# Kernel tuning notes

Measured on AMD Instinct MI355X. Metric: run time of the kernel, lower is better.

## Reference

```python
import jax, jax.numpy as jnp
import numpy as np

B, F, D = 16384, 32, 64   # batch, n_continuous_features, input_dim
H = 2 * D                  # hidden = 2*input_dim per the d_hidden spec


def setup_inputs() -> dict:
    key = jax.random.key(0)
    ks = jax.random.split(key, 6)
    s1 = 1.0 / np.sqrt(D).astype(np.float32)
    s2 = 1.0 / np.sqrt(H).astype(np.float32)
    return {
        "X": jax.random.normal(ks[0], (B, F), jnp.float32),
        "r_": jax.random.normal(ks[1], (B, F, D), jnp.float32),
        # stacked per-feature weights (one tiny MLP per continuous column)
        "W1": jax.random.normal(ks[2], (F, D, H), jnp.float32) * s1,
        "b1": jax.random.normal(ks[3], (F, H), jnp.float32) * s1,
        "W2": jax.random.normal(ks[4], (F, H, 1), jnp.float32) * s2,
        "b2": jax.random.normal(ks[5], (F, 1), jnp.float32) * s2,
    }


def reference(X, r_, W1, b1, W2, b2):
    # Per-feature 2-layer MLP (Linear->relu->Linear->relu), batched over the
    # feature axis instead of the original Python loop over ModuleDict.
    h = jax.nn.relu(jnp.einsum('bfd,fdh->bfh', r_, W1) + b1)   # [B,F,H]
    y = jax.nn.relu(jnp.einsum('bfh,fho->bfo', h, W2) + b2)    # [B,F,1]
    x = X[..., None]                                           # [B,F,1] raw scalar per column
    # Original returns list of (x_col, mlp_out) pairs; we pack them as [B,F,2]
    # with [...,0]=x and [...,1]=mlp output (same values, dense layout).
    return jnp.concatenate([x, y], axis=-1)
```

## Files before the change

### kernel.cpp

```cpp
#include <hip/hip_runtime.h>
#include <stdint.h>

#define B_SZ 16384
#define F_SZ 32
#define D_SZ 64
#define H_SZ 128
#define RSTRIDE 72

typedef __attribute__((ext_vector_type(8))) short  short8;
typedef __attribute__((ext_vector_type(4))) float  float4v;
typedef __attribute__((ext_vector_type(4))) unsigned int uint4v;

__device__ __forceinline__ unsigned int pkbf(float lo, float hi) {
  unsigned int ulo = __builtin_bit_cast(unsigned int, lo) + 0x8000u;
  unsigned int uhi = __builtin_bit_cast(unsigned int, hi) + 0x8000u;
  return __builtin_amdgcn_perm(uhi, ulo, 0x07060302u);
}

__global__ __launch_bounds__(256) void ContMlp_prep(
    const float* __restrict__ W1, const float* __restrict__ b1,
    const float* __restrict__ W2, unsigned short* __restrict__ w1t,
    unsigned int* __restrict__ bw) {
  const int f  = blockIdx.x >> 2;
  const int hq = blockIdx.x & 3;
  const int h0 = hq * 32;
  const int t  = threadIdx.x;
  __shared__ float lds[D_SZ][33];
  const float* w1f = W1 + (size_t)f * (D_SZ * H_SZ);
#pragma unroll
  for (int i = 0; i < 8; ++i) {
    int idx = t + 256 * i;
    int d = idx >> 5, hh = idx & 31;
    lds[d][hh] = w1f[d * H_SZ + h0 + hh];
  }
  __syncthreads();
  unsigned short* o = w1t + (size_t)f * (H_SZ * D_SZ);
#pragma unroll
  for (int i = 0; i < 8; ++i) {
    int idx = t + 256 * i;
    int hh = idx >> 6, d = idx & 63;
    unsigned int u = __builtin_bit_cast(unsigned int, lds[d][hh]) + 0x8000u;
    o[(h0 + hh) * D_SZ + d] = (unsigned short)(u >> 16);
  }
  if (hq == 0 && t < H_SZ) {
    unsigned int ub = __builtin_bit_cast(unsigned int, b1[f * H_SZ + t]) + 0x8000u;
    unsigned int uw = __builtin_bit_cast(unsigned int, W2[f * H_SZ + t]) + 0x8000u;
    bw[f * H_SZ + t] = (ub & 0xFFFF0000u) | (uw >> 16);
  }
}

__global__ __launch_bounds__(256) void ContMlp_main(
    const float* __restrict__ r_,
    const unsigned short* __restrict__ w1t, const unsigned int* __restrict__ bw,
    const float* __restrict__ b2, float* __restrict__ ydst,
    int y_fmul, int y_rmul, int y_cadd) {
  const int f    = blockIdx.x & 31;
  const int tile = blockIdx.x >> 5;
  const int w    = threadIdx.x >> 6;
  const int l    = threadIdx.x & 63;
  const int col  = l & 15;
  const int quad = l >> 4;

  __shared__ unsigned short w1l[H_SZ * RSTRIDE];
  __shared__ unsigned int   bwl[H_SZ];
  __shared__ float          rbuf[4][1024];

  {
    const uint4v* src = (const uint4v*)(w1t + (size_t)f * (H_SZ * D_SZ));
#pragma unroll
    for (int i = 0; i < 4; ++i) {
      int ci = threadIdx.x + 256 * i;
      int h = ci >> 3, dc = ci & 7;
      *(uint4v*)(w1l + h * RSTRIDE + dc * 8) = src[ci];
    }
    if (threadIdx.x < H_SZ) bwl[threadIdx.x] = bw[f * H_SZ + threadIdx.x];
  }
  __syncthreads();
  const float b2f = b2[f];

  const int row_w0 = tile * 512 + w * 128;
  const float* gl = r_ + (size_t)(row_w0 + col) * (F_SZ * D_SZ)
                       + f * D_SZ + quad * 4;
  float* rb = &rbuf[w][0];
  float yv[8];

#pragma unroll 1
  for (int s = 0; s < 8; ++s) {
    const float* gs = gl + (size_t)s * 16 * (F_SZ * D_SZ);
#pragma unroll
    for (int i = 0; i < 4; ++i) {
      __builtin_amdgcn_global_load_lds(
          (const __attribute__((address_space(1))) void*)(gs + i * 16),
          (__attribute__((address_space(3))) void*)(rb + i * 256),
          16, 0, 0);
    }
    __builtin_amdgcn_s_waitcnt(0x0F70);

    float4v f0 = *(const float4v*)(rb + (quad * 2) * 64 + col * 4);
    float4v f1 = *(const float4v*)(rb + (quad * 2 + 1) * 64 + col * 4);
    float4v f2 = *(const float4v*)(rb + (8 + quad * 2) * 64 + col * 4);
    float4v f3 = *(const float4v*)(rb + (9 + quad * 2) * 64 + col * 4);
    uint4v bq0 = {pkbf(f0.x, f0.y), pkbf(f0.z, f0.w),
                  pkbf(f1.x, f1.y), pkbf(f1.z, f1.w)};
    uint4v bq1 = {pkbf(f2.x, f2.y), pkbf(f2.z, f2.w),
                  pkbf(f3.x, f3.y), pkbf(f3.z, f3.w)};
    short8 bf0 = __builtin_bit_cast(short8, bq0);
    short8 bf1 = __builtin_bit_cast(short8, bq1);

    float ysum = 0.f;
#pragma unroll
    for (int t = 0; t < 8; ++t) {
      const unsigned short* wrow = w1l + (col + 16 * t) * RSTRIDE + quad * 8;
      short8 a0 = *(const short8*)(wrow);
      short8 a1 = *(const short8*)(wrow + 32);
      float4v acc = {0.f, 0.f, 0.f, 0.f};
      acc = __builtin_amdgcn_mfma_f32_16x16x32_bf16(a0, bf0, acc, 0, 0, 0);
      acc = __builtin_amdgcn_mfma_f32_16x16x32_bf16(a1, bf1, acc, 0, 0, 0);
      uint4v bwv = *(const uint4v*)(bwl + 16 * t + quad * 4);
#pragma unroll
      for (int r = 0; r < 4; ++r) {
        unsigned int u = bwv[r];
        float b1v = __builtin_bit_cast(float, u & 0xFFFF0000u);
        float w2v = __builtin_bit_cast(float, u << 16);
        ysum = fmaf(fmaxf(acc[r] + b1v, 0.f), w2v, ysum);
      }
    }
    ysum += __shfl_xor(ysum, 16, 64);
    ysum += __shfl_xor(ysum, 32, 64);
    yv[s] = fmaxf(ysum + b2f, 0.f);
  }

  if (quad == 0) {
#pragma unroll
    for (int s = 0; s < 8; ++s) {
      float* yp = ydst + (size_t)f * y_fmul
                       + (size_t)(row_w0 + s * 16 + col) * y_rmul + y_cadd;
      *yp = yv[s];
    }
  }
}

__global__ __launch_bounds__(256) void ContMlp_combine(
    const float* __restrict__ X, const float* __restrict__ yws,
    float* __restrict__ out) {
  __shared__ float yl[F_SZ][33];
  const int r0 = blockIdx.x * 32;
  const int t = threadIdx.x;
#pragma unroll
  for (int i = 0; i < 4; ++i) {
    int idx = t + 256 * i;
    int f = idx >> 5, r = idx & 31;
    yl[f][r] = yws[(size_t)f * B_SZ + r0 + r];
  }
  __syncthreads();
#pragma unroll
  for (int i = 0; i < 4; ++i) {
    int idx = t + 256 * i;
    int r = idx >> 5, f = idx & 31;
    float2 o2 = make_float2(X[(size_t)(r0 + r) * F_SZ + f], yl[f][r]);
    *(float2*)(out + (size_t)(r0 + r) * (2 * F_SZ) + 2 * f) = o2;
  }
}

__global__ __launch_bounds__(256) void ContMlp_xwrite(
    const float* __restrict__ X, float* __restrict__ out) {
  int idx = blockIdx.x * 256 + threadIdx.x;
  int r = idx >> 5, f = idx & 31;
  out[(size_t)r * (2 * F_SZ) + 2 * f] = X[idx];
}

extern "C" void kernel_launch(void* const* d_in, const int* in_sizes, int n_in,
                              void* d_out, int out_size, void* d_ws, size_t ws_size,
                              hipStream_t stream) {
  const float* X  = (const float*)d_in[0];
  const float* r_ = (const float*)d_in[1];
  const float* W1 = (const float*)d_in[2];
  const float* b1 = (const float*)d_in[3];
  const float* W2 = (const float*)d_in[4];
  const float* b2 = (const float*)d_in[5];
  float* out = (float*)d_out;

  const size_t w1t_bytes = (size_t)F_SZ * H_SZ * D_SZ * 2;
  const size_t bw_off    = w1t_bytes;
  const size_t bw_bytes  = (size_t)F_SZ * H_SZ * 4;
  const size_t y_off     = bw_off + bw_bytes;
  const size_t y_bytes   = (size_t)B_SZ * F_SZ * 4;

  unsigned short* w1t = (unsigned short*)d_ws;
  unsigned int*   bw  = (unsigned int*)((char*)d_ws + bw_off);

  ContMlp_prep<<<F_SZ * 4, 256, 0, stream>>>(W1, b1, W2, w1t, bw);

  if (ws_size >= y_off + y_bytes) {
    float* yws = (float*)((char*)d_ws + y_off);
    ContMlp_main<<<32 * F_SZ, 256, 0, stream>>>(r_, w1t, bw, b2, yws,
                                                B_SZ, 1, 0);
    ContMlp_combine<<<B_SZ / 32, 256, 0, stream>>>(X, yws, out);
  } else {
    ContMlp_main<<<32 * F_SZ, 256, 0, stream>>>(r_, w1t, bw, b2, out,
                                                2, 2 * F_SZ, 1);
    ContMlp_xwrite<<<(B_SZ * F_SZ) / 256, 256, 0, stream>>>(X, out);
  }
}
```

Measured before the change: 214.4 us.

## Fuse weight prep, MLP, and output interleave into a single kernel

Merges the three kernels (weight transpose/bf16 pack, per-feature MLP, and X/y interleave) into one launch. Each block now transposes and packs its feature's W1 slice into LDS itself, reusing the r-buffer as scratch, and writes the interleaved (x, y) pairs straight to the output. This removes two extra launches and the workspace round trip for y. In exchange every block repeats the W1 transpose for its feature (32x redundant weight reads and conversion work), adds extra barriers, and the final writes are strided float2 stores. Block indexing also changes from feature-minor to feature-major ordering.

```diff
diff --git a/kernel.cpp b/kernel.cpp
--- a/kernel.cpp
+++ b/kernel.cpp
@@ -17,45 +17,13 @@
   return __builtin_amdgcn_perm(uhi, ulo, 0x07060302u);
 }
 
-__global__ __launch_bounds__(256) void ContMlp_prep(
+__global__ __launch_bounds__(256) void ContMlp_fused(
+    const float* __restrict__ X, const float* __restrict__ r_,
     const float* __restrict__ W1, const float* __restrict__ b1,
-    const float* __restrict__ W2, unsigned short* __restrict__ w1t,
-    unsigned int* __restrict__ bw) {
-  const int f  = blockIdx.x >> 2;
-  const int hq = blockIdx.x & 3;
-  const int h0 = hq * 32;
-  const int t  = threadIdx.x;
-  __shared__ float lds[D_SZ][33];
-  const float* w1f = W1 + (size_t)f * (D_SZ * H_SZ);
-#pragma unroll
-  for (int i = 0; i < 8; ++i) {
-    int idx = t + 256 * i;
-    int d = idx >> 5, hh = idx & 31;
-    lds[d][hh] = w1f[d * H_SZ + h0 + hh];
-  }
-  __syncthreads();
-  unsigned short* o = w1t + (size_t)f * (H_SZ * D_SZ);
-#pragma unroll
-  for (int i = 0; i < 8; ++i) {
-    int idx = t + 256 * i;
-    int hh = idx >> 6, d = idx & 63;
-    unsigned int u = __builtin_bit_cast(unsigned int, lds[d][hh]) + 0x8000u;
-    o[(h0 + hh) * D_SZ + d] = (unsigned short)(u >> 16);
-  }
-  if (hq == 0 && t < H_SZ) {
-    unsigned int ub = __builtin_bit_cast(unsigned int, b1[f * H_SZ + t]) + 0x8000u;
-    unsigned int uw = __builtin_bit_cast(unsigned int, W2[f * H_SZ + t]) + 0x8000u;
-    bw[f * H_SZ + t] = (ub & 0xFFFF0000u) | (uw >> 16);
-  }
-}
-
-__global__ __launch_bounds__(256) void ContMlp_main(
-    const float* __restrict__ r_,
-    const unsigned short* __restrict__ w1t, const unsigned int* __restrict__ bw,
-    const float* __restrict__ b2, float* __restrict__ ydst,
-    int y_fmul, int y_rmul, int y_cadd) {
-  const int f    = blockIdx.x & 31;
-  const int tile = blockIdx.x >> 5;
+    const float* __restrict__ W2, const float* __restrict__ b2,
+    float* __restrict__ out) {
+  const int f    = blockIdx.x >> 5;
+  const int tile = blockIdx.x & 31;
   const int w    = threadIdx.x >> 6;
   const int l    = threadIdx.x & 63;
   const int col  = l & 15;
@@ -66,16 +34,33 @@
   __shared__ float          rbuf[4][1024];
 
   {
-    const uint4v* src = (const uint4v*)(w1t + (size_t)f * (H_SZ * D_SZ));
+    const float* w1f = W1 + (size_t)f * (D_SZ * H_SZ);
+    float (*tmp)[33] = (float (*)[33])&rbuf[0][0];
+    for (int hq = 0; hq < 4; ++hq) {
+      const int h0 = hq * 32;
+      __syncthreads();
 #pragma unroll
-    for (int i = 0; i < 4; ++i) {
-      int ci = threadIdx.x + 256 * i;
-      int h = ci >> 3, dc = ci & 7;
-      *(uint4v*)(w1l + h * RSTRIDE + dc * 8) = src[ci];
+      for (int i = 0; i < 8; ++i) {
+        int idx = threadIdx.x + 256 * i;
+        int d = idx >> 5, hh = idx & 31;
+        tmp[d][hh] = w1f[d * H_SZ + h0 + hh];
+      }
+      __syncthreads();
+#pragma unroll
+      for (int i = 0; i < 4; ++i) {
+        int idx = threadIdx.x + 256 * i;
+        int hh = idx & 31, dp = idx >> 5;
+        unsigned int v = pkbf(tmp[2 * dp][hh], tmp[2 * dp + 1][hh]);
+        *(unsigned int*)(w1l + (h0 + hh) * RSTRIDE + 2 * dp) = v;
+      }
     }
-    if (threadIdx.x < H_SZ) bwl[threadIdx.x] = bw[f * H_SZ + threadIdx.x];
+    if (threadIdx.x < H_SZ) {
+      unsigned int ub = __builtin_bit_cast(unsigned int, b1[f * H_SZ + threadIdx.x]) + 0x8000u;
+      unsigned int uw = __builtin_bit_cast(unsigned int, W2[f * H_SZ + threadIdx.x]) + 0x8000u;
+      bwl[threadIdx.x] = (ub & 0xFFFF0000u) | (uw >> 16);
+    }
+    __syncthreads();
   }
-  __syncthreads();
   const float b2f = b2[f];
 
   const int row_w0 = tile * 512 + w * 128;
@@ -133,40 +118,11 @@
   if (quad == 0) {
 #pragma unroll
     for (int s = 0; s < 8; ++s) {
-      float* yp = ydst + (size_t)f * y_fmul
-                       + (size_t)(row_w0 + s * 16 + col) * y_rmul + y_cadd;
-      *yp = yv[s];
+      int row = row_w0 + s * 16 + col;
+      float xv = X[(size_t)row * F_SZ + f];
+      *(float2*)(out + (size_t)row * (2 * F_SZ) + 2 * f) = make_float2(xv, yv[s]);
     }
   }
-}
-
-__global__ __launch_bounds__(256) void ContMlp_combine(
-    const float* __restrict__ X, const float* __restrict__ yws,
-    float* __restrict__ out) {
-  __shared__ float yl[F_SZ][33];
-  const int r0 = blockIdx.x * 32;
-  const int t = threadIdx.x;
-#pragma unroll
-  for (int i = 0; i < 4; ++i) {
-    int idx = t + 256 * i;
-    int f = idx >> 5, r = idx & 31;
-    yl[f][r] = yws[(size_t)f * B_SZ + r0 + r];
-  }
-  __syncthreads();
-#pragma unroll
-  for (int i = 0; i < 4; ++i) {
-    int idx = t + 256 * i;
-    int r = idx >> 5, f = idx & 31;
-    float2 o2 = make_float2(X[(size_t)(r0 + r) * F_SZ + f], yl[f][r]);
-    *(float2*)(out + (size_t)(r0 + r) * (2 * F_SZ) + 2 * f) = o2;
-  }
-}
-
-__global__ __launch_bounds__(256) void ContMlp_xwrite(
-    const float* __restrict__ X, float* __restrict__ out) {
-  int idx = blockIdx.x * 256 + threadIdx.x;
-  int r = idx >> 5, f = idx & 31;
-  out[(size_t)r * (2 * F_SZ) + 2 * f] = X[idx];
 }
 
 extern "C" void kernel_launch(void* const* d_in, const int* in_sizes, int n_in,
@@ -179,26 +135,7 @@
   const float* W2 = (const float*)d_in[4];
   const float* b2 = (const float*)d_in[5];
   float* out = (float*)d_out;
+  (void)d_ws; (void)ws_size;
 
-  const size_t w1t_bytes = (size_t)F_SZ * H_SZ * D_SZ * 2;
-  const size_t bw_off    = w1t_bytes;
-  const size_t bw_bytes  = (size_t)F_SZ * H_SZ * 4;
-  const size_t y_off     = bw_off + bw_bytes;
-  const size_t y_bytes   = (size_t)B_SZ * F_SZ * 4;
-
-  unsigned short* w1t = (unsigned short*)d_ws;
-  unsigned int*   bw  = (unsigned int*)((char*)d_ws + bw_off);
-
-  ContMlp_prep<<<F_SZ * 4, 256, 0, stream>>>(W1, b1, W2, w1t, bw);
-
-  if (ws_size >= y_off + y_bytes) {
-    float* yws = (float*)((char*)d_ws + y_off);
-    ContMlp_main<<<32 * F_SZ, 256, 0, stream>>>(r_, w1t, bw, b2, yws,
-                                                B_SZ, 1, 0);
-    ContMlp_combine<<<B_SZ / 32, 256, 0, stream>>>(X, yws, out);
-  } else {
-    ContMlp_main<<<32 * F_SZ, 256, 0, stream>>>(r_, w1t, bw, b2, out,
-                                                2, 2 * F_SZ, 1);
-    ContMlp_xwrite<<<(B_SZ * F_SZ) / 256, 256, 0, stream>>>(X, out);
-  }
+  ContMlp_fused<<<F_SZ * 32, 256, 0, stream>>>(X, r_, W1, b1, W2, b2, out);
 }
```

Measured after the change: 215.4 us. No clear change (+0.5%).
